# Kernel optimization log

Measured on AMD Instinct MI355X. Metric: run time of the kernel, lower is better.

The kernel has to match this reference:

```python
import jax, jax.numpy as jnp
import numpy as np


def setup_inputs() -> dict:
    key = jax.random.key(0)
    ks = jax.random.split(key, 4)
    B, T, I, H, O = 1024, 512, 64, 128, 10
    return {
        "x": jax.random.normal(ks[0], (B, T, I), dtype=jnp.float32),
        "W_hx": jax.random.normal(ks[1], (H, I), dtype=jnp.float32) * (6.0 / (H + I)) ** 0.5,
        "W_hh": jax.random.normal(ks[2], (H, H), dtype=jnp.float32) * (6.0 / (H + H)) ** 0.5,
        "b_hh": jnp.zeros((H,), dtype=jnp.float32),
        "W_ph": jax.random.normal(ks[3], (O, H), dtype=jnp.float32) * (6.0 / (O + H)) ** 0.5,
        "b_ph": jnp.zeros((O,), dtype=jnp.float32),
    }


def reference(x, W_hx, W_hh, b_hh, W_ph, b_ph):
    B, T, I = x.shape
    H = W_hh.shape[0]
    # Precompute input projections for all timesteps in one GEMM: [B,T,H]
    xproj = jnp.einsum("bti,hi->bth", x, W_hx)
    h0 = jnp.zeros((B, H), dtype=x.dtype)

    def step(h, xp_t):
        # xp_t: [B,H]; recurrent update h = tanh(W_hx x_t + W_hh h + b)
        h_new = jnp.tanh(xp_t + h @ W_hh.T + b_hh)
        return h_new, None

    # scan over time (leading axis): xproj transposed to [T,B,H]
    h_T, _ = jax.lax.scan(step, h0, jnp.swapaxes(xproj, 0, 1))
    return h_T @ W_ph.T + b_ph
```

## Files before the change

kernel.cpp:

```cpp
#include <hip/hip_runtime.h>
#include <math.h>


#define T_STEPS 512
#define I_DIM   64
#define H_DIM   128
#define O_DIM   10
#define BT      16
#define PITCH   136

typedef short  bf16x8 __attribute__((ext_vector_type(8)));
typedef float  f32x4  __attribute__((ext_vector_type(4)));

#define MFMA(A, Bi, C) __builtin_amdgcn_mfma_f32_16x16x32_bf16((A), __builtin_bit_cast(bf16x8, (Bi)), (C), 0, 0, 0)

static __device__ inline short f2bf(float f) {
    union { float f; unsigned u; } v; v.f = f;
    unsigned r = v.u + 0x7FFFu + ((v.u >> 16) & 1u);
    return (short)(r >> 16);
}
static __device__ inline unsigned rbf(float f) {
    return (__builtin_bit_cast(unsigned, f) + 0x8000u) >> 16;
}
static __device__ inline int pk2(float a, float b) {
    unsigned ua = __builtin_bit_cast(unsigned, a);
    unsigned ub = __builtin_bit_cast(unsigned, b);
    return (int)(((ua + 0x8000u) >> 16) | ((ub + 0x8000u) & 0xFFFF0000u));
}
static __device__ inline float bf2f(short s) {
    union { unsigned u; float f; } v; v.u = ((unsigned)(unsigned short)s) << 16;
    return v.f;
}

static __device__ inline void lds_barrier() {
    asm volatile("s_waitcnt lgkmcnt(0)\n\ts_barrier" ::: "memory");
}

#define RNN_STEP(P, XR, TN)                                                     \
    {                                                                           \
        const short* hb = hbuf[P] + c * PITCH + q * 8;                          \
        bf16x8 Ah0 = *(const bf16x8*)(hb +  0);                                 \
        bf16x8 Ah1 = *(const bf16x8*)(hb + 32);                                 \
        bf16x8 Ah2 = *(const bf16x8*)(hb + 64);                                 \
        bf16x8 Ah3 = *(const bf16x8*)(hb + 96);                                 \
        f32x4 Ca0 = Cxa0, Cb0 = Cxb0, Ca1 = Cxa1, Cb1 = Cxb1;                   \
        Ca0 = MFMA(Ah0, Bw[0][0], Ca0); Ca1 = MFMA(Ah0, Bw[1][0], Ca1);         \
        Cb0 = MFMA(Ah1, Bw[0][1], Cb0); Cb1 = MFMA(Ah1, Bw[1][1], Cb1);         \
        Ca0 = MFMA(Ah2, Bw[0][2], Ca0); Ca1 = MFMA(Ah2, Bw[1][2], Ca1);         \
        Cb0 = MFMA(Ah3, Bw[0][3], Cb0); Cb1 = MFMA(Ah3, Bw[1][3], Cb1);         \
        const f32x4 C0 = Ca0 + Cb0;                                             \
        const f32x4 C1 = Ca1 + Cb1;                                             \
        short* hw = hbuf[1 - (P)];                                              \
        _Pragma("unroll")                                                       \
        for (int r = 0; r < 4; ++r) {                                           \
            const int m = q * 4 + r;                                            \
            float s0 = C0[r] + bias0, s1 = C1[r] + bias1;                       \
            float e0 = __builtin_amdgcn_exp2f(s0 * 2.885390081777926825f);      \
            float e1 = __builtin_amdgcn_exp2f(s1 * 2.885390081777926825f);      \
            float h0 = fmaf(-2.0f, __builtin_amdgcn_rcpf(e0 + 1.0f), 1.0f);     \
            float h1 = fmaf(-2.0f, __builtin_amdgcn_rcpf(e1 + 1.0f), 1.0f);     \
            hw[m * PITCH + w * 32 + c]      = (short)rbf(h0);                   \
            hw[m * PITCH + w * 32 + 16 + c] = (short)rbf(h1);                   \
        }                                                                       \
         \
        {                                                                       \
            int4 axi0, axi1;                                                    \
            axi0.x = pk2(XR[0].x, XR[0].y); axi0.y = pk2(XR[0].z, XR[0].w);     \
            axi0.z = pk2(XR[1].x, XR[1].y); axi0.w = pk2(XR[1].z, XR[1].w);     \
            axi1.x = pk2(XR[2].x, XR[2].y); axi1.y = pk2(XR[2].z, XR[2].w);     \
            axi1.z = pk2(XR[3].x, XR[3].y); axi1.w = pk2(XR[3].z, XR[3].w);     \
            const int tn = ((TN) < T_STEPS) ? (TN) : (T_STEPS - 1);             \
            const float* pn = xrow + (size_t)tn * I_DIM;                        \
            XR[0] = *(const float4*)(pn +      q * 8);                          \
            XR[1] = *(const float4*)(pn +      q * 8 + 4);                      \
            XR[2] = *(const float4*)(pn + 32 + q * 8);                          \
            XR[3] = *(const float4*)(pn + 32 + q * 8 + 4);                      \
            bf16x8 Ax0 = __builtin_bit_cast(bf16x8, axi0);                      \
            bf16x8 Ax1 = __builtin_bit_cast(bf16x8, axi1);                      \
            const f32x4 Z = {0.f, 0.f, 0.f, 0.f};                               \
            Cxa0 = MFMA(Ax0, Bw[0][4], Z);                                      \
            Cxb0 = MFMA(Ax1, Bw[0][5], Z);                                      \
            Cxa1 = MFMA(Ax0, Bw[1][4], Z);                                      \
            Cxb1 = MFMA(Ax1, Bw[1][5], Z);                                      \
        }                                                                       \
        lds_barrier();                                                          \
    }

__global__ __launch_bounds__(256)
__attribute__((amdgpu_waves_per_eu(1, 2)))
void rnn_mfma_kernel(
    const float* __restrict__ x,
    const float* __restrict__ W_hx,
    const float* __restrict__ W_hh,
    const float* __restrict__ b_hh,
    const float* __restrict__ W_ph,
    const float* __restrict__ b_ph,
    float* __restrict__ out)
{
    const int b0   = blockIdx.x * BT;
    const int tid  = threadIdx.x;
    const int w    = tid >> 6;
    const int lane = tid & 63;
    const int c    = lane & 15;
    const int q    = lane >> 4;

    __shared__ short hbuf[2][BT * PITCH];

    int4 Bw[2][6];
    #pragma unroll
    for (int nt = 0; nt < 2; ++nt) {
        const int n = w * 32 + nt * 16 + c;
        #pragma unroll
        for (int kt = 0; kt < 6; ++kt) {
            const float* src = (kt < 4) ? (W_hh + n * H_DIM + kt * 32 + q * 8)
                                        : (W_hx + n * I_DIM + (kt - 4) * 32 + q * 8);
            short e[8];
            #pragma unroll
            for (int j = 0; j < 8; ++j) e[j] = f2bf(src[j]);
            Bw[nt][kt].x = ((int)(unsigned short)e[0]) | ((int)(unsigned short)e[1] << 16);
            Bw[nt][kt].y = ((int)(unsigned short)e[2]) | ((int)(unsigned short)e[3] << 16);
            Bw[nt][kt].z = ((int)(unsigned short)e[4]) | ((int)(unsigned short)e[5] << 16);
            Bw[nt][kt].w = ((int)(unsigned short)e[6]) | ((int)(unsigned short)e[7] << 16);
        }
    }
    #pragma unroll
    for (int nt = 0; nt < 2; ++nt)
        #pragma unroll
        for (int kt = 0; kt < 6; ++kt)
            asm volatile("" : "+v"(Bw[nt][kt].x), "+v"(Bw[nt][kt].y),
                              "+v"(Bw[nt][kt].z), "+v"(Bw[nt][kt].w));

    const float bias0 = b_hh[w * 32 + c];
    const float bias1 = b_hh[w * 32 + 16 + c];

    for (int idx = tid; idx < BT * PITCH; idx += 256) hbuf[0][idx] = 0;

    const float* xrow = x + (size_t)(b0 + c) * T_STEPS * I_DIM;
    float4 xrA[4], xrB[4];
    {
        const float* p0 = xrow;
        xrA[0] = *(const float4*)(p0 +      q * 8);
        xrA[1] = *(const float4*)(p0 +      q * 8 + 4);
        xrA[2] = *(const float4*)(p0 + 32 + q * 8);
        xrA[3] = *(const float4*)(p0 + 32 + q * 8 + 4);
        const float* p1 = xrow + I_DIM;
        xrB[0] = *(const float4*)(p1 +      q * 8);
        xrB[1] = *(const float4*)(p1 +      q * 8 + 4);
        xrB[2] = *(const float4*)(p1 + 32 + q * 8);
        xrB[3] = *(const float4*)(p1 + 32 + q * 8 + 4);
    }

    f32x4 Cxa0, Cxb0, Cxa1, Cxb1;
    {
        int4 axi0, axi1;
        axi0.x = pk2(xrA[0].x, xrA[0].y); axi0.y = pk2(xrA[0].z, xrA[0].w);
        axi0.z = pk2(xrA[1].x, xrA[1].y); axi0.w = pk2(xrA[1].z, xrA[1].w);
        axi1.x = pk2(xrA[2].x, xrA[2].y); axi1.y = pk2(xrA[2].z, xrA[2].w);
        axi1.z = pk2(xrA[3].x, xrA[3].y); axi1.w = pk2(xrA[3].z, xrA[3].w);
        const float* p2 = xrow + 2 * I_DIM;
        xrA[0] = *(const float4*)(p2 +      q * 8);
        xrA[1] = *(const float4*)(p2 +      q * 8 + 4);
        xrA[2] = *(const float4*)(p2 + 32 + q * 8);
        xrA[3] = *(const float4*)(p2 + 32 + q * 8 + 4);
        bf16x8 Ax0 = __builtin_bit_cast(bf16x8, axi0);
        bf16x8 Ax1 = __builtin_bit_cast(bf16x8, axi1);
        const f32x4 Z = {0.f, 0.f, 0.f, 0.f};
        Cxa0 = MFMA(Ax0, Bw[0][4], Z);
        Cxb0 = MFMA(Ax1, Bw[0][5], Z);
        Cxa1 = MFMA(Ax0, Bw[1][4], Z);
        Cxb1 = MFMA(Ax1, Bw[1][5], Z);
    }
    __syncthreads();

    #pragma unroll 1
    for (int t = 0; t < T_STEPS; t += 2) {
        RNN_STEP(0, xrB, t + 3)
        RNN_STEP(1, xrA, t + 4)
    }

    if (tid < BT * O_DIM) {
        const int m = tid / O_DIM;
        const int o = tid % O_DIM;
        float acc = b_ph[o];
        #pragma unroll 4
        for (int k = 0; k < H_DIM; ++k)
            acc = fmaf(W_ph[o * H_DIM + k], bf2f(hbuf[0][m * PITCH + k]), acc);
        out[(size_t)(b0 + m) * O_DIM + o] = acc;
    }
}

extern "C" void kernel_launch(void* const* d_in, const int* in_sizes, int n_in,
                              void* d_out, int out_size, void* d_ws, size_t ws_size,
                              hipStream_t stream) {
    const float* x    = (const float*)d_in[0];
    const float* W_hx = (const float*)d_in[1];
    const float* W_hh = (const float*)d_in[2];
    const float* b_hh = (const float*)d_in[3];
    const float* W_ph = (const float*)d_in[4];
    const float* b_ph = (const float*)d_in[5];
    float* out = (float*)d_out;

    rnn_mfma_kernel<<<1024 / BT, 256, 0, stream>>>(x, W_hx, W_hh, b_hh, W_ph, b_ph, out);
}
```

Before: 513.3 us.

## Split recurrence into producer/consumer waves and use Pade tanh

Doubles the block to 512 threads. Four producer waves load x, convert it to bf16 and compute the input projection plus bias with MFMA into a double-buffered LDS buffer one step ahead. Four consumer waves run only the recurrent W_hh MFMAs and the tanh, at raised priority. The tanh becomes a clamped Pade rational and the hidden-state stores are packed into pairs with a changed column mapping. This takes global loads and the input GEMM off the serial critical path, at the cost of extra LDS traffic and a larger barrier group, with the Pade approximation adding accuracy risk.

After: 463.6 us. 1.11x faster.

```diff
diff --git a/kernel.cpp b/kernel.cpp
--- a/kernel.cpp
+++ b/kernel.cpp
@@ -8,6 +8,7 @@
 #define O_DIM   10
 #define BT      16
 #define PITCH   136
+#define XPITCH  20
 
 typedef short  bf16x8 __attribute__((ext_vector_type(8)));
 typedef float  f32x4  __attribute__((ext_vector_type(4)));
@@ -19,9 +20,6 @@
     unsigned r = v.u + 0x7FFFu + ((v.u >> 16) & 1u);
     return (short)(r >> 16);
 }
-static __device__ inline unsigned rbf(float f) {
-    return (__builtin_bit_cast(unsigned, f) + 0x8000u) >> 16;
-}
 static __device__ inline int pk2(float a, float b) {
     unsigned ua = __builtin_bit_cast(unsigned, a);
     unsigned ub = __builtin_bit_cast(unsigned, b);
@@ -31,19 +29,39 @@
     union { unsigned u; float f; } v; v.u = ((unsigned)(unsigned short)s) << 16;
     return v.f;
 }
-
+static __device__ inline float pade_tanh(float z) {
+    const float t = z * z;
+    const float p = fmaf(fmaf(t + 378.0f, t, 17325.0f), t, 135135.0f);
+    const float qd = fmaf(fmaf(fmaf(28.0f, t, 3150.0f), t, 62370.0f), t, 135135.0f);
+    const float r = (z * p) * __builtin_amdgcn_rcpf(qd);
+    return __builtin_amdgcn_fmed3f(r, -1.0f, 1.0f);
+}
 static __device__ inline void lds_barrier() {
     asm volatile("s_waitcnt lgkmcnt(0)\n\ts_barrier" ::: "memory");
 }
-
-#define RNN_STEP(P, XR, TN)                                                     \
+static __device__ inline int4 load_frag(const float* src) {
+    short e[8];
+    #pragma unroll
+    for (int j = 0; j < 8; ++j) e[j] = f2bf(src[j]);
+    int4 r;
+    r.x = ((int)(unsigned short)e[0]) | ((int)(unsigned short)e[1] << 16);
+    r.y = ((int)(unsigned short)e[2]) | ((int)(unsigned short)e[3] << 16);
+    r.z = ((int)(unsigned short)e[4]) | ((int)(unsigned short)e[5] << 16);
+    r.w = ((int)(unsigned short)e[6]) | ((int)(unsigned short)e[7] << 16);
+    return r;
+}
+
+#define CONS_STEP(P)                                                            \
     {                                                                           \
         const short* hb = hbuf[P] + c * PITCH + q * 8;                          \
         bf16x8 Ah0 = *(const bf16x8*)(hb +  0);                                 \
         bf16x8 Ah1 = *(const bf16x8*)(hb + 32);                                 \
         bf16x8 Ah2 = *(const bf16x8*)(hb + 64);                                 \
         bf16x8 Ah3 = *(const bf16x8*)(hb + 96);                                 \
-        f32x4 Ca0 = Cxa0, Cb0 = Cxb0, Ca1 = Cxa1, Cb1 = Cxb1;                   \
+        f32x4 Ca0 = *(const f32x4*)&xpb[P][ n0      * XPITCH + 4 * q];          \
+        f32x4 Ca1 = *(const f32x4*)&xpb[P][(n0 + 1) * XPITCH + 4 * q];          \
+        f32x4 Cb0 = {0.f, 0.f, 0.f, 0.f};                                       \
+        f32x4 Cb1 = {0.f, 0.f, 0.f, 0.f};                                       \
         Ca0 = MFMA(Ah0, Bw[0][0], Ca0); Ca1 = MFMA(Ah0, Bw[1][0], Ca1);         \
         Cb0 = MFMA(Ah1, Bw[0][1], Cb0); Cb1 = MFMA(Ah1, Bw[1][1], Cb1);         \
         Ca0 = MFMA(Ah2, Bw[0][2], Ca0); Ca1 = MFMA(Ah2, Bw[1][2], Ca1);         \
@@ -54,40 +72,36 @@
         _Pragma("unroll")                                                       \
         for (int r = 0; r < 4; ++r) {                                           \
             const int m = q * 4 + r;                                            \
-            float s0 = C0[r] + bias0, s1 = C1[r] + bias1;                       \
-            float e0 = __builtin_amdgcn_exp2f(s0 * 2.885390081777926825f);      \
-            float e1 = __builtin_amdgcn_exp2f(s1 * 2.885390081777926825f);      \
-            float h0 = fmaf(-2.0f, __builtin_amdgcn_rcpf(e0 + 1.0f), 1.0f);     \
-            float h1 = fmaf(-2.0f, __builtin_amdgcn_rcpf(e1 + 1.0f), 1.0f);     \
-            hw[m * PITCH + w * 32 + c]      = (short)rbf(h0);                   \
-            hw[m * PITCH + w * 32 + 16 + c] = (short)rbf(h1);                   \
+            const float h0 = pade_tanh(C0[r]);                                  \
+            const float h1 = pade_tanh(C1[r]);                                  \
+            *(int*)(hw + m * PITCH + n0) = pk2(h0, h1);                         \
         }                                                                       \
-         \
-        {                                                                       \
-            int4 axi0, axi1;                                                    \
-            axi0.x = pk2(XR[0].x, XR[0].y); axi0.y = pk2(XR[0].z, XR[0].w);     \
-            axi0.z = pk2(XR[1].x, XR[1].y); axi0.w = pk2(XR[1].z, XR[1].w);     \
-            axi1.x = pk2(XR[2].x, XR[2].y); axi1.y = pk2(XR[2].z, XR[2].w);     \
-            axi1.z = pk2(XR[3].x, XR[3].y); axi1.w = pk2(XR[3].z, XR[3].w);     \
-            const int tn = ((TN) < T_STEPS) ? (TN) : (T_STEPS - 1);             \
-            const float* pn = xrow + (size_t)tn * I_DIM;                        \
-            XR[0] = *(const float4*)(pn +      q * 8);                          \
-            XR[1] = *(const float4*)(pn +      q * 8 + 4);                      \
-            XR[2] = *(const float4*)(pn + 32 + q * 8);                          \
-            XR[3] = *(const float4*)(pn + 32 + q * 8 + 4);                      \
-            bf16x8 Ax0 = __builtin_bit_cast(bf16x8, axi0);                      \
-            bf16x8 Ax1 = __builtin_bit_cast(bf16x8, axi1);                      \
-            const f32x4 Z = {0.f, 0.f, 0.f, 0.f};                               \
-            Cxa0 = MFMA(Ax0, Bw[0][4], Z);                                      \
-            Cxb0 = MFMA(Ax1, Bw[0][5], Z);                                      \
-            Cxa1 = MFMA(Ax0, Bw[1][4], Z);                                      \
-            Cxb1 = MFMA(Ax1, Bw[1][5], Z);                                      \
-        }                                                                       \
-        lds_barrier();                                                          \
-    }
-
-__global__ __launch_bounds__(256)
-__attribute__((amdgpu_waves_per_eu(1, 2)))
+    }
+
+#define PROD_STEP(P, XR, TN)                                                    \
+    {                                                                           \
+        int4 a0, a1;                                                            \
+        a0.x = pk2(XR[0].x, XR[0].y); a0.y = pk2(XR[0].z, XR[0].w);             \
+        a0.z = pk2(XR[1].x, XR[1].y); a0.w = pk2(XR[1].z, XR[1].w);             \
+        a1.x = pk2(XR[2].x, XR[2].y); a1.y = pk2(XR[2].z, XR[2].w);             \
+        a1.z = pk2(XR[3].x, XR[3].y); a1.w = pk2(XR[3].z, XR[3].w);             \
+        const int tn = ((TN) < T_STEPS) ? (TN) : (T_STEPS - 1);                 \
+        const float* pn = xrow + (size_t)tn * I_DIM;                            \
+        XR[0] = *(const float4*)(pn +      q * 8);                              \
+        XR[1] = *(const float4*)(pn +      q * 8 + 4);                          \
+        XR[2] = *(const float4*)(pn + 32 + q * 8);                              \
+        XR[3] = *(const float4*)(pn + 32 + q * 8 + 4);                          \
+        bf16x8 Ax0 = __builtin_bit_cast(bf16x8, a0);                            \
+        bf16x8 Ax1 = __builtin_bit_cast(bf16x8, a1);                            \
+        f32x4 P0 = MFMA(Ax0, BX[0][0], biasv[0]);                               \
+        P0 = MFMA(Ax1, BX[0][1], P0);                                           \
+        f32x4 P1 = MFMA(Ax0, BX[1][0], biasv[1]);                               \
+        P1 = MFMA(Ax1, BX[1][1], P1);                                           \
+        *(f32x4*)&xpb[1 - (P)][ n0      * XPITCH + 4 * q] = P0;                 \
+        *(f32x4*)&xpb[1 - (P)][(n0 + 1) * XPITCH + 4 * q] = P1;                 \
+    }
+
+__global__ __launch_bounds__(512, 2)
 void rnn_mfma_kernel(
     const float* __restrict__ x,
     const float* __restrict__ W_hx,
@@ -99,83 +113,99 @@
 {
     const int b0   = blockIdx.x * BT;
     const int tid  = threadIdx.x;
-    const int w    = tid >> 6;
+    const int wave = tid >> 6;
     const int lane = tid & 63;
     const int c    = lane & 15;
     const int q    = lane >> 4;
-
-    __shared__ short hbuf[2][BT * PITCH];
-
-    int4 Bw[2][6];
-    #pragma unroll
-    for (int nt = 0; nt < 2; ++nt) {
-        const int n = w * 32 + nt * 16 + c;
-        #pragma unroll
-        for (int kt = 0; kt < 6; ++kt) {
-            const float* src = (kt < 4) ? (W_hh + n * H_DIM + kt * 32 + q * 8)
-                                        : (W_hx + n * I_DIM + (kt - 4) * 32 + q * 8);
-            short e[8];
-            #pragma unroll
-            for (int j = 0; j < 8; ++j) e[j] = f2bf(src[j]);
-            Bw[nt][kt].x = ((int)(unsigned short)e[0]) | ((int)(unsigned short)e[1] << 16);
-            Bw[nt][kt].y = ((int)(unsigned short)e[2]) | ((int)(unsigned short)e[3] << 16);
-            Bw[nt][kt].z = ((int)(unsigned short)e[4]) | ((int)(unsigned short)e[5] << 16);
-            Bw[nt][kt].w = ((int)(unsigned short)e[6]) | ((int)(unsigned short)e[7] << 16);
-        }
-    }
-    #pragma unroll
-    for (int nt = 0; nt < 2; ++nt)
-        #pragma unroll
-        for (int kt = 0; kt < 6; ++kt)
-            asm volatile("" : "+v"(Bw[nt][kt].x), "+v"(Bw[nt][kt].y),
-                              "+v"(Bw[nt][kt].z), "+v"(Bw[nt][kt].w));
-
-    const float bias0 = b_hh[w * 32 + c];
-    const float bias1 = b_hh[w * 32 + 16 + c];
-
-    for (int idx = tid; idx < BT * PITCH; idx += 256) hbuf[0][idx] = 0;
-
-    const float* xrow = x + (size_t)(b0 + c) * T_STEPS * I_DIM;
-    float4 xrA[4], xrB[4];
-    {
-        const float* p0 = xrow;
-        xrA[0] = *(const float4*)(p0 +      q * 8);
-        xrA[1] = *(const float4*)(p0 +      q * 8 + 4);
-        xrA[2] = *(const float4*)(p0 + 32 + q * 8);
-        xrA[3] = *(const float4*)(p0 + 32 + q * 8 + 4);
+    const int w    = wave & 3;
+    const int n0   = w * 32 + 2 * c;
+
+    __shared__ __align__(16) short hbuf[2][BT * PITCH];
+    __shared__ __align__(16) float xpb[2][H_DIM * XPITCH];
+
+    for (int idx = tid; idx < BT * PITCH; idx += 512) hbuf[0][idx] = 0;
+
+    if (wave < 4) {
+        int4 Bw[2][4];
+        #pragma unroll
+        for (int nt = 0; nt < 2; ++nt)
+            #pragma unroll
+            for (int kt = 0; kt < 4; ++kt)
+                Bw[nt][kt] = load_frag(W_hh + (n0 + nt) * H_DIM + kt * 32 + q * 8);
+        #pragma unroll
+        for (int nt = 0; nt < 2; ++nt)
+            #pragma unroll
+            for (int kt = 0; kt < 4; ++kt)
+                asm volatile("" : "+v"(Bw[nt][kt].x), "+v"(Bw[nt][kt].y),
+                                  "+v"(Bw[nt][kt].z), "+v"(Bw[nt][kt].w));
+        __syncthreads();
+        __builtin_amdgcn_s_setprio(1);
+        #pragma unroll 1
+        for (int t = 0; t < T_STEPS; t += 2) {
+            CONS_STEP(0)
+            lds_barrier();
+            CONS_STEP(1)
+            lds_barrier();
+        }
+        __builtin_amdgcn_s_setprio(0);
+    } else {
+        int4 BX[2][2];
+        f32x4 biasv[2];
+        #pragma unroll
+        for (int nt = 0; nt < 2; ++nt) {
+            #pragma unroll
+            for (int kx = 0; kx < 2; ++kx)
+                BX[nt][kx] = load_frag(W_hx + (n0 + nt) * I_DIM + kx * 32 + q * 8);
+            const float bb = b_hh[n0 + nt];
+            biasv[nt] = (f32x4){bb, bb, bb, bb};
+        }
+        #pragma unroll
+        for (int nt = 0; nt < 2; ++nt)
+            #pragma unroll
+            for (int kx = 0; kx < 2; ++kx)
+                asm volatile("" : "+v"(BX[nt][kx].x), "+v"(BX[nt][kx].y),
+                                  "+v"(BX[nt][kx].z), "+v"(BX[nt][kx].w));
+
+        const float* xrow = x + (size_t)(b0 + c) * T_STEPS * I_DIM;
+        {
+            float4 x0[4];
+            x0[0] = *(const float4*)(xrow +      q * 8);
+            x0[1] = *(const float4*)(xrow +      q * 8 + 4);
+            x0[2] = *(const float4*)(xrow + 32 + q * 8);
+            x0[3] = *(const float4*)(xrow + 32 + q * 8 + 4);
+            int4 a0, a1;
+            a0.x = pk2(x0[0].x, x0[0].y); a0.y = pk2(x0[0].z, x0[0].w);
+            a0.z = pk2(x0[1].x, x0[1].y); a0.w = pk2(x0[1].z, x0[1].w);
+            a1.x = pk2(x0[2].x, x0[2].y); a1.y = pk2(x0[2].z, x0[2].w);
+            a1.z = pk2(x0[3].x, x0[3].y); a1.w = pk2(x0[3].z, x0[3].w);
+            bf16x8 Ax0 = __builtin_bit_cast(bf16x8, a0);
+            bf16x8 Ax1 = __builtin_bit_cast(bf16x8, a1);
+            f32x4 P0 = MFMA(Ax0, BX[0][0], biasv[0]);
+            P0 = MFMA(Ax1, BX[0][1], P0);
+            f32x4 P1 = MFMA(Ax0, BX[1][0], biasv[1]);
+            P1 = MFMA(Ax1, BX[1][1], P1);
+            *(f32x4*)&xpb[0][ n0      * XPITCH + 4 * q] = P0;
+            *(f32x4*)&xpb[0][(n0 + 1) * XPITCH + 4 * q] = P1;
+        }
+        float4 xrA[4], xrB[4];
         const float* p1 = xrow + I_DIM;
-        xrB[0] = *(const float4*)(p1 +      q * 8);
-        xrB[1] = *(const float4*)(p1 +      q * 8 + 4);
-        xrB[2] = *(const float4*)(p1 + 32 + q * 8);
-        xrB[3] = *(const float4*)(p1 + 32 + q * 8 + 4);
-    }
-
-    f32x4 Cxa0, Cxb0, Cxa1, Cxb1;
-    {
-        int4 axi0, axi1;
-        axi0.x = pk2(xrA[0].x, xrA[0].y); axi0.y = pk2(xrA[0].z, xrA[0].w);
-        axi0.z = pk2(xrA[1].x, xrA[1].y); axi0.w = pk2(xrA[1].z, xrA[1].w);
-        axi1.x = pk2(xrA[2].x, xrA[2].y); axi1.y = pk2(xrA[2].z, xrA[2].w);
-        axi1.z = pk2(xrA[3].x, xrA[3].y); axi1.w = pk2(xrA[3].z, xrA[3].w);
+        xrA[0] = *(const float4*)(p1 +      q * 8);
+        xrA[1] = *(const float4*)(p1 +      q * 8 + 4);
+        xrA[2] = *(const float4*)(p1 + 32 + q * 8);
+        xrA[3] = *(const float4*)(p1 + 32 + q * 8 + 4);
         const float* p2 = xrow + 2 * I_DIM;
-        xrA[0] = *(const float4*)(p2 +      q * 8);
-        xrA[1] = *(const float4*)(p2 +      q * 8 + 4);
-        xrA[2] = *(const float4*)(p2 + 32 + q * 8);
-        xrA[3] = *(const float4*)(p2 + 32 + q * 8 + 4);
-        bf16x8 Ax0 = __builtin_bit_cast(bf16x8, axi0);
-        bf16x8 Ax1 = __builtin_bit_cast(bf16x8, axi1);
-        const f32x4 Z = {0.f, 0.f, 0.f, 0.f};
-        Cxa0 = MFMA(Ax0, Bw[0][4], Z);
-        Cxb0 = MFMA(Ax1, Bw[0][5], Z);
-        Cxa1 = MFMA(Ax0, Bw[1][4], Z);
-        Cxb1 = MFMA(Ax1, Bw[1][5], Z);
-    }
-    __syncthreads();
-
-    #pragma unroll 1
-    for (int t = 0; t < T_STEPS; t += 2) {
-        RNN_STEP(0, xrB, t + 3)
-        RNN_STEP(1, xrA, t + 4)
+        xrB[0] = *(const float4*)(p2 +      q * 8);
+        xrB[1] = *(const float4*)(p2 +      q * 8 + 4);
+        xrB[2] = *(const float4*)(p2 + 32 + q * 8);
+        xrB[3] = *(const float4*)(p2 + 32 + q * 8 + 4);
+        __syncthreads();
+        #pragma unroll 1
+        for (int t = 0; t < T_STEPS; t += 2) {
+            PROD_STEP(0, xrA, t + 3)
+            lds_barrier();
+            PROD_STEP(1, xrB, t + 4)
+            lds_barrier();
+        }
     }
 
     if (tid < BT * O_DIM) {
@@ -200,5 +230,5 @@
     const float* b_ph = (const float*)d_in[5];
     float* out = (float*)d_out;
 
-    rnn_mfma_kernel<<<1024 / BT, 256, 0, stream>>>(x, W_hx, W_hh, b_hh, W_ph, b_ph, out);
-}
+    rnn_mfma_kernel<<<1024 / BT, 512, 0, stream>>>(x, W_hx, W_hh, b_hh, W_ph, b_ph, out);
+}
```

## Run each batch tile's recurrence in one wave without barriers

Applied to the files above, without the earlier changes.

Each 16-row batch tile is now handled by a single 64-lane wave instead of four waves. That one wave holds all 128 hidden columns of W_hh and W_hx as bf16 register fragments and runs the whole 48-MFMA step itself. This removes the per-step workgroup barrier and the double-buffered LDS hidden state, leaving one buffer and an lgkmcnt wait. Bias is folded into the MFMA accumulator init, and hidden outputs are interleaved so each lane writes packed bf16 pairs. The cost is that the matrix work and tanh work per step are serialized on one SIMD with very high register use.

New measurement: 806.5 us. 1.57x slower.

```diff
diff --git a/kernel.cpp b/kernel.cpp
--- a/kernel.cpp
+++ b/kernel.cpp
@@ -12,16 +12,14 @@
 typedef short  bf16x8 __attribute__((ext_vector_type(8)));
 typedef float  f32x4  __attribute__((ext_vector_type(4)));
 
-#define MFMA(A, Bi, C) __builtin_amdgcn_mfma_f32_16x16x32_bf16((A), __builtin_bit_cast(bf16x8, (Bi)), (C), 0, 0, 0)
+#define MFMA(A, Bi, C) __builtin_amdgcn_mfma_f32_16x16x32_bf16(                 \
+    __builtin_bit_cast(bf16x8, (A)), __builtin_bit_cast(bf16x8, (Bi)), (C), 0, 0, 0)
 
 static __device__ inline short f2bf(float f) {
     union { float f; unsigned u; } v; v.f = f;
     unsigned r = v.u + 0x7FFFu + ((v.u >> 16) & 1u);
     return (short)(r >> 16);
 }
-static __device__ inline unsigned rbf(float f) {
-    return (__builtin_bit_cast(unsigned, f) + 0x8000u) >> 16;
-}
 static __device__ inline int pk2(float a, float b) {
     unsigned ua = __builtin_bit_cast(unsigned, a);
     unsigned ub = __builtin_bit_cast(unsigned, b);
@@ -31,63 +29,78 @@
     union { unsigned u; float f; } v; v.u = ((unsigned)(unsigned short)s) << 16;
     return v.f;
 }
-
-static __device__ inline void lds_barrier() {
-    asm volatile("s_waitcnt lgkmcnt(0)\n\ts_barrier" ::: "memory");
-}
-
-#define RNN_STEP(P, XR, TN)                                                     \
+static __device__ inline float tanh_fast(float z) {
+    float e = __builtin_amdgcn_exp2f(z * 2.885390081777926825f);
+    return fmaf(-2.0f, __builtin_amdgcn_rcpf(e + 1.0f), 1.0f);
+}
+static __device__ inline int4 load_frag(const float* src) {
+    short e[8];
+    #pragma unroll
+    for (int j = 0; j < 8; ++j) e[j] = f2bf(src[j]);
+    int4 r;
+    r.x = ((int)(unsigned short)e[0]) | ((int)(unsigned short)e[1] << 16);
+    r.y = ((int)(unsigned short)e[2]) | ((int)(unsigned short)e[3] << 16);
+    r.z = ((int)(unsigned short)e[4]) | ((int)(unsigned short)e[5] << 16);
+    r.w = ((int)(unsigned short)e[6]) | ((int)(unsigned short)e[7] << 16);
+    return r;
+}
+static __device__ inline void lds_fence() {
+    asm volatile("s_waitcnt lgkmcnt(0)" ::: "memory");
+    __builtin_amdgcn_sched_barrier(0);
+}
+
+#define RNN_STEP(XR, TN)                                                        \
     {                                                                           \
-        const short* hb = hbuf[P] + c * PITCH + q * 8;                          \
+        const short* hb = hbuf + c * PITCH + q * 8;                             \
         bf16x8 Ah0 = *(const bf16x8*)(hb +  0);                                 \
         bf16x8 Ah1 = *(const bf16x8*)(hb + 32);                                 \
         bf16x8 Ah2 = *(const bf16x8*)(hb + 64);                                 \
         bf16x8 Ah3 = *(const bf16x8*)(hb + 96);                                 \
-        f32x4 Ca0 = Cxa0, Cb0 = Cxb0, Ca1 = Cxa1, Cb1 = Cxb1;                   \
-        Ca0 = MFMA(Ah0, Bw[0][0], Ca0); Ca1 = MFMA(Ah0, Bw[1][0], Ca1);         \
-        Cb0 = MFMA(Ah1, Bw[0][1], Cb0); Cb1 = MFMA(Ah1, Bw[1][1], Cb1);         \
-        Ca0 = MFMA(Ah2, Bw[0][2], Ca0); Ca1 = MFMA(Ah2, Bw[1][2], Ca1);         \
-        Cb0 = MFMA(Ah3, Bw[0][3], Cb0); Cb1 = MFMA(Ah3, Bw[1][3], Cb1);         \
-        const f32x4 C0 = Ca0 + Cb0;                                             \
-        const f32x4 C1 = Ca1 + Cb1;                                             \
-        short* hw = hbuf[1 - (P)];                                              \
+        f32x4 C[4][2];                                                          \
         _Pragma("unroll")                                                       \
-        for (int r = 0; r < 4; ++r) {                                           \
-            const int m = q * 4 + r;                                            \
-            float s0 = C0[r] + bias0, s1 = C1[r] + bias1;                       \
-            float e0 = __builtin_amdgcn_exp2f(s0 * 2.885390081777926825f);      \
-            float e1 = __builtin_amdgcn_exp2f(s1 * 2.885390081777926825f);      \
-            float h0 = fmaf(-2.0f, __builtin_amdgcn_rcpf(e0 + 1.0f), 1.0f);     \
-            float h1 = fmaf(-2.0f, __builtin_amdgcn_rcpf(e1 + 1.0f), 1.0f);     \
-            hw[m * PITCH + w * 32 + c]      = (short)rbf(h0);                   \
-            hw[m * PITCH + w * 32 + 16 + c] = (short)rbf(h1);                   \
+        for (int np = 0; np < 4; ++np) {                                        \
+            _Pragma("unroll")                                                   \
+            for (int sub = 0; sub < 2; ++sub) {                                 \
+                C[np][sub] = MFMA(AXF[0], BW[np][sub][4], biasC4[np][sub]);     \
+                C[np][sub] = MFMA(AXF[1], BW[np][sub][5], C[np][sub]);          \
+                C[np][sub] = MFMA(Ah0, BW[np][sub][0], C[np][sub]);             \
+                C[np][sub] = MFMA(Ah1, BW[np][sub][1], C[np][sub]);             \
+                C[np][sub] = MFMA(Ah2, BW[np][sub][2], C[np][sub]);             \
+                C[np][sub] = MFMA(Ah3, BW[np][sub][3], C[np][sub]);             \
+            }                                                                   \
         }                                                                       \
-         \
+        _Pragma("unroll")                                                       \
+        for (int np = 0; np < 4; ++np) {                                        \
+            _Pragma("unroll")                                                   \
+            for (int r = 0; r < 4; ++r) {                                       \
+                const int m = q * 4 + r;                                        \
+                const float h0 = tanh_fast(C[np][0][r]);                        \
+                const float h1 = tanh_fast(C[np][1][r]);                        \
+                *(int*)(hbuf + m * PITCH + 32 * np + 2 * c) = pk2(h0, h1);      \
+            }                                                                   \
+        }                                                                       \
+        lds_fence();                                                            \
+        AXF[0] = pack4(XR[0], XR[1]);                                           \
+        AXF[1] = pack4(XR[2], XR[3]);                                           \
         {                                                                       \
-            int4 axi0, axi1;                                                    \
-            axi0.x = pk2(XR[0].x, XR[0].y); axi0.y = pk2(XR[0].z, XR[0].w);     \
-            axi0.z = pk2(XR[1].x, XR[1].y); axi0.w = pk2(XR[1].z, XR[1].w);     \
-            axi1.x = pk2(XR[2].x, XR[2].y); axi1.y = pk2(XR[2].z, XR[2].w);     \
-            axi1.z = pk2(XR[3].x, XR[3].y); axi1.w = pk2(XR[3].z, XR[3].w);     \
             const int tn = ((TN) < T_STEPS) ? (TN) : (T_STEPS - 1);             \
             const float* pn = xrow + (size_t)tn * I_DIM;                        \
             XR[0] = *(const float4*)(pn +      q * 8);                          \
             XR[1] = *(const float4*)(pn +      q * 8 + 4);                      \
             XR[2] = *(const float4*)(pn + 32 + q * 8);                          \
             XR[3] = *(const float4*)(pn + 32 + q * 8 + 4);                      \
-            bf16x8 Ax0 = __builtin_bit_cast(bf16x8, axi0);                      \
-            bf16x8 Ax1 = __builtin_bit_cast(bf16x8, axi1);                      \
-            const f32x4 Z = {0.f, 0.f, 0.f, 0.f};                               \
-            Cxa0 = MFMA(Ax0, Bw[0][4], Z);                                      \
-            Cxb0 = MFMA(Ax1, Bw[0][5], Z);                                      \
-            Cxa1 = MFMA(Ax0, Bw[1][4], Z);                                      \
-            Cxb1 = MFMA(Ax1, Bw[1][5], Z);                                      \
         }                                                                       \
-        lds_barrier();                                                          \
-    }
-
-__global__ __launch_bounds__(256)
-__attribute__((amdgpu_waves_per_eu(1, 2)))
+    }
+
+static __device__ inline int4 pack4(const float4 a, const float4 b) {
+    int4 r;
+    r.x = pk2(a.x, a.y); r.y = pk2(a.z, a.w);
+    r.z = pk2(b.x, b.y); r.w = pk2(b.z, b.w);
+    return r;
+}
+
+__global__ __launch_bounds__(64, 1)
+__attribute__((amdgpu_waves_per_eu(1, 1)))
 void rnn_mfma_kernel(
     const float* __restrict__ x,
     const float* __restrict__ W_hx,
@@ -99,92 +112,81 @@
 {
     const int b0   = blockIdx.x * BT;
     const int tid  = threadIdx.x;
-    const int w    = tid >> 6;
     const int lane = tid & 63;
     const int c    = lane & 15;
     const int q    = lane >> 4;
 
-    __shared__ short hbuf[2][BT * PITCH];
-
-    int4 Bw[2][6];
+    __shared__ __align__(16) short hbuf[BT * PITCH];
+
+    int4 BW[4][2][6];
+    f32x4 biasC4[4][2];
     #pragma unroll
-    for (int nt = 0; nt < 2; ++nt) {
-        const int n = w * 32 + nt * 16 + c;
+    for (int np = 0; np < 4; ++np) {
         #pragma unroll
-        for (int kt = 0; kt < 6; ++kt) {
-            const float* src = (kt < 4) ? (W_hh + n * H_DIM + kt * 32 + q * 8)
-                                        : (W_hx + n * I_DIM + (kt - 4) * 32 + q * 8);
-            short e[8];
+        for (int sub = 0; sub < 2; ++sub) {
+            const int n = 32 * np + 2 * c + sub;
             #pragma unroll
-            for (int j = 0; j < 8; ++j) e[j] = f2bf(src[j]);
-            Bw[nt][kt].x = ((int)(unsigned short)e[0]) | ((int)(unsigned short)e[1] << 16);
-            Bw[nt][kt].y = ((int)(unsigned short)e[2]) | ((int)(unsigned short)e[3] << 16);
-            Bw[nt][kt].z = ((int)(unsigned short)e[4]) | ((int)(unsigned short)e[5] << 16);
-            Bw[nt][kt].w = ((int)(unsigned short)e[6]) | ((int)(unsigned short)e[7] << 16);
+            for (int kt = 0; kt < 6; ++kt) {
+                const float* src = (kt < 4) ? (W_hh + n * H_DIM + kt * 32 + q * 8)
+                                            : (W_hx + n * I_DIM + (kt - 4) * 32 + q * 8);
+                BW[np][sub][kt] = load_frag(src);
+            }
+            const float bb = b_hh[n];
+            biasC4[np][sub] = (f32x4){bb, bb, bb, bb};
         }
     }
     #pragma unroll
-    for (int nt = 0; nt < 2; ++nt)
+    for (int np = 0; np < 4; ++np)
         #pragma unroll
-        for (int kt = 0; kt < 6; ++kt)
-            asm volatile("" : "+v"(Bw[nt][kt].x), "+v"(Bw[nt][kt].y),
-                              "+v"(Bw[nt][kt].z), "+v"(Bw[nt][kt].w));
-
-    const float bias0 = b_hh[w * 32 + c];
-    const float bias1 = b_hh[w * 32 + 16 + c];
-
-    for (int idx = tid; idx < BT * PITCH; idx += 256) hbuf[0][idx] = 0;
+        for (int sub = 0; sub < 2; ++sub) {
+            #pragma unroll
+            for (int kt = 0; kt < 6; ++kt)
+                asm volatile("" : "+v"(BW[np][sub][kt].x), "+v"(BW[np][sub][kt].y),
+                                  "+v"(BW[np][sub][kt].z), "+v"(BW[np][sub][kt].w));
+            asm volatile("" : "+v"(biasC4[np][sub]));
+        }
+
+    for (int idx = tid; idx < BT * PITCH; idx += 64) hbuf[idx] = 0;
+    lds_fence();
 
     const float* xrow = x + (size_t)(b0 + c) * T_STEPS * I_DIM;
+    int4 AXF[2];
+    {
+        float4 x0[4];
+        x0[0] = *(const float4*)(xrow +      q * 8);
+        x0[1] = *(const float4*)(xrow +      q * 8 + 4);
+        x0[2] = *(const float4*)(xrow + 32 + q * 8);
+        x0[3] = *(const float4*)(xrow + 32 + q * 8 + 4);
+        AXF[0] = pack4(x0[0], x0[1]);
+        AXF[1] = pack4(x0[2], x0[3]);
+    }
     float4 xrA[4], xrB[4];
     {
-        const float* p0 = xrow;
-        xrA[0] = *(const float4*)(p0 +      q * 8);
-        xrA[1] = *(const float4*)(p0 +      q * 8 + 4);
-        xrA[2] = *(const float4*)(p0 + 32 + q * 8);
-        xrA[3] = *(const float4*)(p0 + 32 + q * 8 + 4);
         const float* p1 = xrow + I_DIM;
-        xrB[0] = *(const float4*)(p1 +      q * 8);
-        xrB[1] = *(const float4*)(p1 +      q * 8 + 4);
-        xrB[2] = *(const float4*)(p1 + 32 + q * 8);
-        xrB[3] = *(const float4*)(p1 + 32 + q * 8 + 4);
-    }
-
-    f32x4 Cxa0, Cxb0, Cxa1, Cxb1;
-    {
-        int4 axi0, axi1;
-        axi0.x = pk2(xrA[0].x, xrA[0].y); axi0.y = pk2(xrA[0].z, xrA[0].w);
-        axi0.z = pk2(xrA[1].x, xrA[1].y); axi0.w = pk2(xrA[1].z, xrA[1].w);
-        axi1.x = pk2(xrA[2].x, xrA[2].y); axi1.y = pk2(xrA[2].z, xrA[2].w);
-        axi1.z = pk2(xrA[3].x, xrA[3].y); axi1.w = pk2(xrA[3].z, xrA[3].w);
+        xrA[0] = *(const float4*)(p1 +      q * 8);
+        xrA[1] = *(const float4*)(p1 +      q * 8 + 4);
+        xrA[2] = *(const float4*)(p1 + 32 + q * 8);
+        xrA[3] = *(const float4*)(p1 + 32 + q * 8 + 4);
         const float* p2 = xrow + 2 * I_DIM;
-        xrA[0] = *(const float4*)(p2 +      q * 8);
-        xrA[1] = *(const float4*)(p2 +      q * 8 + 4);
-        xrA[2] = *(const float4*)(p2 + 32 + q * 8);
-        xrA[3] = *(const float4*)(p2 + 32 + q * 8 + 4);
-        bf16x8 Ax0 = __builtin_bit_cast(bf16x8, axi0);
-        bf16x8 Ax1 = __builtin_bit_cast(bf16x8, axi1);
-        const f32x4 Z = {0.f, 0.f, 0.f, 0.f};
-        Cxa0 = MFMA(Ax0, Bw[0][4], Z);
-        Cxb0 = MFMA(Ax1, Bw[0][5], Z);
-        Cxa1 = MFMA(Ax0, Bw[1][4], Z);
-        Cxb1 = MFMA(Ax1, Bw[1][5], Z);
-    }
-    __syncthreads();
+        xrB[0] = *(const float4*)(p2 +      q * 8);
+        xrB[1] = *(const float4*)(p2 +      q * 8 + 4);
+        xrB[2] = *(const float4*)(p2 + 32 + q * 8);
+        xrB[3] = *(const float4*)(p2 + 32 + q * 8 + 4);
+    }
 
     #pragma unroll 1
     for (int t = 0; t < T_STEPS; t += 2) {
-        RNN_STEP(0, xrB, t + 3)
-        RNN_STEP(1, xrA, t + 4)
-    }
-
-    if (tid < BT * O_DIM) {
-        const int m = tid / O_DIM;
-        const int o = tid % O_DIM;
+        RNN_STEP(xrA, t + 3)
+        RNN_STEP(xrB, t + 4)
+    }
+
+    for (int idx = tid; idx < BT * O_DIM; idx += 64) {
+        const int m = idx / O_DIM;
+        const int o = idx % O_DIM;
         float acc = b_ph[o];
         #pragma unroll 4
         for (int k = 0; k < H_DIM; ++k)
-            acc = fmaf(W_ph[o * H_DIM + k], bf2f(hbuf[0][m * PITCH + k]), acc);
+            acc = fmaf(W_ph[o * H_DIM + k], bf2f(hbuf[m * PITCH + k]), acc);
         out[(size_t)(b0 + m) * O_DIM + o] = acc;
     }
 }
@@ -200,5 +202,5 @@
     const float* b_ph = (const float*)d_in[5];
     float* out = (float*)d_out;
 
-    rnn_mfma_kernel<<<1024 / BT, 256, 0, stream>>>(x, W_hx, W_hh, b_hh, W_ph, b_ph, out);
-}
+    rnn_mfma_kernel<<<1024 / BT, 64, 0, stream>>>(x, W_hx, W_hh, b_hh, W_ph, b_ph, out);
+}
```

## Pack two batch chunks per block, use rational tanh and packed h stores

Applied to the files above, without the earlier changes.

Each block now runs two independent 16-row batch chunks with 8 waves, which halves the grid to 32 blocks of 512 threads sharing one barrier per step. Tanh is replaced by a Padé rational approximation clamped with med3, using a single reciprocal shared by two outputs instead of two exp2 and two rcp. The column mapping is permuted so each lane writes two adjacent bf16 h values as one packed 32-bit LDS store. The bias is folded into the input-projection MFMA accumulator. Halving the block count leaves more CUs idle, the shared barrier couples the two chunks, and the Padé form loses accuracy for larger pre-activations.

New measurement: 657.5 us. +28.1%, slower.

```diff
diff --git a/kernel.cpp b/kernel.cpp
--- a/kernel.cpp
+++ b/kernel.cpp
@@ -7,21 +7,20 @@
 #define H_DIM   128
 #define O_DIM   10
 #define BT      16
+#define NCH     2
 #define PITCH   136
 
 typedef short  bf16x8 __attribute__((ext_vector_type(8)));
 typedef float  f32x4  __attribute__((ext_vector_type(4)));
 
-#define MFMA(A, Bi, C) __builtin_amdgcn_mfma_f32_16x16x32_bf16((A), __builtin_bit_cast(bf16x8, (Bi)), (C), 0, 0, 0)
+#define MFMA(A, Bi, C) __builtin_amdgcn_mfma_f32_16x16x32_bf16(                 \
+    __builtin_bit_cast(bf16x8, (A)), __builtin_bit_cast(bf16x8, (Bi)), (C), 0, 0, 0)
 
 static __device__ inline short f2bf(float f) {
     union { float f; unsigned u; } v; v.f = f;
     unsigned r = v.u + 0x7FFFu + ((v.u >> 16) & 1u);
     return (short)(r >> 16);
 }
-static __device__ inline unsigned rbf(float f) {
-    return (__builtin_bit_cast(unsigned, f) + 0x8000u) >> 16;
-}
 static __device__ inline int pk2(float a, float b) {
     unsigned ua = __builtin_bit_cast(unsigned, a);
     unsigned ub = __builtin_bit_cast(unsigned, b);
@@ -31,63 +30,80 @@
     union { unsigned u; float f; } v; v.u = ((unsigned)(unsigned short)s) << 16;
     return v.f;
 }
-
+static __device__ inline int4 load_frag(const float* src) {
+    short e[8];
+    #pragma unroll
+    for (int j = 0; j < 8; ++j) e[j] = f2bf(src[j]);
+    int4 r;
+    r.x = ((int)(unsigned short)e[0]) | ((int)(unsigned short)e[1] << 16);
+    r.y = ((int)(unsigned short)e[2]) | ((int)(unsigned short)e[3] << 16);
+    r.z = ((int)(unsigned short)e[4]) | ((int)(unsigned short)e[5] << 16);
+    r.w = ((int)(unsigned short)e[6]) | ((int)(unsigned short)e[7] << 16);
+    return r;
+}
+static __device__ inline int4 pack4(const float4 a, const float4 b) {
+    int4 r;
+    r.x = pk2(a.x, a.y); r.y = pk2(a.z, a.w);
+    r.z = pk2(b.x, b.y); r.w = pk2(b.z, b.w);
+    return r;
+}
 static __device__ inline void lds_barrier() {
     asm volatile("s_waitcnt lgkmcnt(0)\n\ts_barrier" ::: "memory");
 }
 
 #define RNN_STEP(P, XR, TN)                                                     \
     {                                                                           \
-        const short* hb = hbuf[P] + c * PITCH + q * 8;                          \
+        const short* hb = hsrc[P] + c * PITCH + q * 8;                          \
         bf16x8 Ah0 = *(const bf16x8*)(hb +  0);                                 \
         bf16x8 Ah1 = *(const bf16x8*)(hb + 32);                                 \
         bf16x8 Ah2 = *(const bf16x8*)(hb + 64);                                 \
         bf16x8 Ah3 = *(const bf16x8*)(hb + 96);                                 \
-        f32x4 Ca0 = Cxa0, Cb0 = Cxb0, Ca1 = Cxa1, Cb1 = Cxb1;                   \
-        Ca0 = MFMA(Ah0, Bw[0][0], Ca0); Ca1 = MFMA(Ah0, Bw[1][0], Ca1);         \
-        Cb0 = MFMA(Ah1, Bw[0][1], Cb0); Cb1 = MFMA(Ah1, Bw[1][1], Cb1);         \
-        Ca0 = MFMA(Ah2, Bw[0][2], Ca0); Ca1 = MFMA(Ah2, Bw[1][2], Ca1);         \
-        Cb0 = MFMA(Ah3, Bw[0][3], Cb0); Cb1 = MFMA(Ah3, Bw[1][3], Cb1);         \
+        f32x4 Ca0 = Cx0, Ca1 = Cx1;                                             \
+        f32x4 Cb0 = {0.f, 0.f, 0.f, 0.f};                                       \
+        f32x4 Cb1 = {0.f, 0.f, 0.f, 0.f};                                       \
+        Ca0 = MFMA(Ah0, BW[0][0], Ca0); Ca1 = MFMA(Ah0, BW[1][0], Ca1);         \
+        Cb0 = MFMA(Ah1, BW[0][1], Cb0); Cb1 = MFMA(Ah1, BW[1][1], Cb1);         \
+        Ca0 = MFMA(Ah2, BW[0][2], Ca0); Ca1 = MFMA(Ah2, BW[1][2], Ca1);         \
+        Cb0 = MFMA(Ah3, BW[0][3], Cb0); Cb1 = MFMA(Ah3, BW[1][3], Cb1);         \
         const f32x4 C0 = Ca0 + Cb0;                                             \
         const f32x4 C1 = Ca1 + Cb1;                                             \
-        short* hw = hbuf[1 - (P)];                                              \
+        short* hw = hsrc[1 - (P)];                                              \
         _Pragma("unroll")                                                       \
         for (int r = 0; r < 4; ++r) {                                           \
             const int m = q * 4 + r;                                            \
-            float s0 = C0[r] + bias0, s1 = C1[r] + bias1;                       \
-            float e0 = __builtin_amdgcn_exp2f(s0 * 2.885390081777926825f);      \
-            float e1 = __builtin_amdgcn_exp2f(s1 * 2.885390081777926825f);      \
-            float h0 = fmaf(-2.0f, __builtin_amdgcn_rcpf(e0 + 1.0f), 1.0f);     \
-            float h1 = fmaf(-2.0f, __builtin_amdgcn_rcpf(e1 + 1.0f), 1.0f);     \
-            hw[m * PITCH + w * 32 + c]      = (short)rbf(h0);                   \
-            hw[m * PITCH + w * 32 + 16 + c] = (short)rbf(h1);                   \
+            const float z0 = C0[r], z1 = C1[r];                                 \
+            const float t0 = z0 * z0, t1 = z1 * z1;                             \
+            const float p0 = fmaf(fmaf(t0 + 378.f, t0, 17325.f), t0, 135135.f); \
+            const float p1 = fmaf(fmaf(t1 + 378.f, t1, 17325.f), t1, 135135.f); \
+            const float q0 = fmaf(fmaf(fmaf(28.f, t0, 3150.f), t0, 62370.f), t0, 135135.f); \
+            const float q1 = fmaf(fmaf(fmaf(28.f, t1, 3150.f), t1, 62370.f), t1, 135135.f); \
+            const float rr = __builtin_amdgcn_rcpf(q0 * q1);                    \
+            const float h0 = __builtin_amdgcn_fmed3f(z0 * p0 * (rr * q1), -1.f, 1.f); \
+            const float h1 = __builtin_amdgcn_fmed3f(z1 * p1 * (rr * q0), -1.f, 1.f); \
+            *(int*)(hw + m * PITCH + n0) = pk2(h0, h1);                         \
         }                                                                       \
-         \
+                     \
         {                                                                       \
-            int4 axi0, axi1;                                                    \
-            axi0.x = pk2(XR[0].x, XR[0].y); axi0.y = pk2(XR[0].z, XR[0].w);     \
-            axi0.z = pk2(XR[1].x, XR[1].y); axi0.w = pk2(XR[1].z, XR[1].w);     \
-            axi1.x = pk2(XR[2].x, XR[2].y); axi1.y = pk2(XR[2].z, XR[2].w);     \
-            axi1.z = pk2(XR[3].x, XR[3].y); axi1.w = pk2(XR[3].z, XR[3].w);     \
+            int4 ax0, ax1;                                                      \
+            ax0.x = pk2(XR[0].x, XR[0].y); ax0.y = pk2(XR[0].z, XR[0].w);       \
+            ax0.z = pk2(XR[1].x, XR[1].y); ax0.w = pk2(XR[1].z, XR[1].w);       \
+            ax1.x = pk2(XR[2].x, XR[2].y); ax1.y = pk2(XR[2].z, XR[2].w);       \
+            ax1.z = pk2(XR[3].x, XR[3].y); ax1.w = pk2(XR[3].z, XR[3].w);       \
             const int tn = ((TN) < T_STEPS) ? (TN) : (T_STEPS - 1);             \
             const float* pn = xrow + (size_t)tn * I_DIM;                        \
             XR[0] = *(const float4*)(pn +      q * 8);                          \
             XR[1] = *(const float4*)(pn +      q * 8 + 4);                      \
             XR[2] = *(const float4*)(pn + 32 + q * 8);                          \
             XR[3] = *(const float4*)(pn + 32 + q * 8 + 4);                      \
-            bf16x8 Ax0 = __builtin_bit_cast(bf16x8, axi0);                      \
-            bf16x8 Ax1 = __builtin_bit_cast(bf16x8, axi1);                      \
-            const f32x4 Z = {0.f, 0.f, 0.f, 0.f};                               \
-            Cxa0 = MFMA(Ax0, Bw[0][4], Z);                                      \
-            Cxb0 = MFMA(Ax1, Bw[0][5], Z);                                      \
-            Cxa1 = MFMA(Ax0, Bw[1][4], Z);                                      \
-            Cxb1 = MFMA(Ax1, Bw[1][5], Z);                                      \
+            Cx0 = MFMA(ax0, BW[0][4], biasv[0]);                                \
+            Cx0 = MFMA(ax1, BW[0][5], Cx0);                                     \
+            Cx1 = MFMA(ax0, BW[1][4], biasv[1]);                                \
+            Cx1 = MFMA(ax1, BW[1][5], Cx1);                                     \
         }                                                                       \
         lds_barrier();                                                          \
     }
 
-__global__ __launch_bounds__(256)
-__attribute__((amdgpu_waves_per_eu(1, 2)))
+__global__ __launch_bounds__(512, 2)
 void rnn_mfma_kernel(
     const float* __restrict__ x,
     const float* __restrict__ W_hx,
@@ -97,43 +113,46 @@
     const float* __restrict__ b_ph,
     float* __restrict__ out)
 {
-    const int b0   = blockIdx.x * BT;
     const int tid  = threadIdx.x;
-    const int w    = tid >> 6;
+    const int wave = tid >> 6;
+    const int g    = wave >> 2;
+    const int w    = wave & 3;
     const int lane = tid & 63;
     const int c    = lane & 15;
     const int q    = lane >> 4;
-
-    __shared__ short hbuf[2][BT * PITCH];
-
-    int4 Bw[2][6];
+    const int n0   = w * 32 + 2 * c;
+    const int b0   = blockIdx.x * (BT * NCH) + g * BT;
+
+    __shared__ __align__(16) short hbuf[NCH][2][BT * PITCH];
+    short* hsrc[2] = { hbuf[g][0], hbuf[g][1] };
+
+    int4 BW[2][6];
+    f32x4 biasv[2];
     #pragma unroll
-    for (int nt = 0; nt < 2; ++nt) {
-        const int n = w * 32 + nt * 16 + c;
+    for (int sub = 0; sub < 2; ++sub) {
+        const int n = n0 + sub;
         #pragma unroll
         for (int kt = 0; kt < 6; ++kt) {
             const float* src = (kt < 4) ? (W_hh + n * H_DIM + kt * 32 + q * 8)
                                         : (W_hx + n * I_DIM + (kt - 4) * 32 + q * 8);
-            short e[8];
-            #pragma unroll
-            for (int j = 0; j < 8; ++j) e[j] = f2bf(src[j]);
-            Bw[nt][kt].x = ((int)(unsigned short)e[0]) | ((int)(unsigned short)e[1] << 16);
-            Bw[nt][kt].y = ((int)(unsigned short)e[2]) | ((int)(unsigned short)e[3] << 16);
-            Bw[nt][kt].z = ((int)(unsigned short)e[4]) | ((int)(unsigned short)e[5] << 16);
-            Bw[nt][kt].w = ((int)(unsigned short)e[6]) | ((int)(unsigned short)e[7] << 16);
+            BW[sub][kt] = load_frag(src);
         }
+        const float bb = b_hh[n];
+        biasv[sub] = (f32x4){bb, bb, bb, bb};
     }
     #pragma unroll
-    for (int nt = 0; nt < 2; ++nt)
+    for (int sub = 0; sub < 2; ++sub) {
         #pragma unroll
         for (int kt = 0; kt < 6; ++kt)
-            asm volatile("" : "+v"(Bw[nt][kt].x), "+v"(Bw[nt][kt].y),
-                              "+v"(Bw[nt][kt].z), "+v"(Bw[nt][kt].w));
-
-    const float bias0 = b_hh[w * 32 + c];
-    const float bias1 = b_hh[w * 32 + 16 + c];
-
-    for (int idx = tid; idx < BT * PITCH; idx += 256) hbuf[0][idx] = 0;
+            asm volatile("" : "+v"(BW[sub][kt].x), "+v"(BW[sub][kt].y),
+                              "+v"(BW[sub][kt].z), "+v"(BW[sub][kt].w));
+        asm volatile("" : "+v"(biasv[sub]));
+    }
+
+    for (int idx = tid; idx < NCH * BT * PITCH; idx += 512)
+        hbuf[0][0][idx % (BT * PITCH) + (idx / (BT * PITCH)) * 0] = 0;
+    for (int idx = tid; idx < NCH * 2 * BT * PITCH; idx += 512)
+        ((short*)hbuf)[idx] = 0;
 
     const float* xrow = x + (size_t)(b0 + c) * T_STEPS * I_DIM;
     float4 xrA[4], xrB[4];
@@ -150,25 +169,20 @@
         xrB[3] = *(const float4*)(p1 + 32 + q * 8 + 4);
     }
 
-    f32x4 Cxa0, Cxb0, Cxa1, Cxb1;
+    f32x4 Cx0, Cx1;
     {
-        int4 axi0, axi1;
-        axi0.x = pk2(xrA[0].x, xrA[0].y); axi0.y = pk2(xrA[0].z, xrA[0].w);
-        axi0.z = pk2(xrA[1].x, xrA[1].y); axi0.w = pk2(xrA[1].z, xrA[1].w);
-        axi1.x = pk2(xrA[2].x, xrA[2].y); axi1.y = pk2(xrA[2].z, xrA[2].w);
-        axi1.z = pk2(xrA[3].x, xrA[3].y); axi1.w = pk2(xrA[3].z, xrA[3].w);
+        int4 ax0, ax1;
+        ax0 = pack4(xrA[0], xrA[1]);
+        ax1 = pack4(xrA[2], xrA[3]);
         const float* p2 = xrow + 2 * I_DIM;
         xrA[0] = *(const float4*)(p2 +      q * 8);
         xrA[1] = *(const float4*)(p2 +      q * 8 + 4);
         xrA[2] = *(const float4*)(p2 + 32 + q * 8);
         xrA[3] = *(const float4*)(p2 + 32 + q * 8 + 4);
-        bf16x8 Ax0 = __builtin_bit_cast(bf16x8, axi0);
-        bf16x8 Ax1 = __builtin_bit_cast(bf16x8, axi1);
-        const f32x4 Z = {0.f, 0.f, 0.f, 0.f};
-        Cxa0 = MFMA(Ax0, Bw[0][4], Z);
-        Cxb0 = MFMA(Ax1, Bw[0][5], Z);
-        Cxa1 = MFMA(Ax0, Bw[1][4], Z);
-        Cxb1 = MFMA(Ax1, Bw[1][5], Z);
+        Cx0 = MFMA(ax0, BW[0][4], biasv[0]);
+        Cx0 = MFMA(ax1, BW[0][5], Cx0);
+        Cx1 = MFMA(ax0, BW[1][4], biasv[1]);
+        Cx1 = MFMA(ax1, BW[1][5], Cx1);
     }
     __syncthreads();
 
@@ -178,14 +192,15 @@
         RNN_STEP(1, xrA, t + 4)
     }
 
-    if (tid < BT * O_DIM) {
-        const int m = tid / O_DIM;
-        const int o = tid % O_DIM;
+    if (tid < NCH * BT * O_DIM) {
+        const int m32 = tid / O_DIM;
+        const int o   = tid % O_DIM;
+        const short* hrow = hbuf[m32 >> 4][0] + (m32 & 15) * PITCH;
         float acc = b_ph[o];
         #pragma unroll 4
         for (int k = 0; k < H_DIM; ++k)
-            acc = fmaf(W_ph[o * H_DIM + k], bf2f(hbuf[0][m * PITCH + k]), acc);
-        out[(size_t)(b0 + m) * O_DIM + o] = acc;
+            acc = fmaf(W_ph[o * H_DIM + k], bf2f(hrow[k]), acc);
+        out[(size_t)(blockIdx.x * (BT * NCH) + m32) * O_DIM + o] = acc;
     }
 }
 
@@ -200,5 +215,5 @@
     const float* b_ph = (const float*)d_in[5];
     float* out = (float*)d_out;
 
-    rnn_mfma_kernel<<<1024 / BT, 256, 0, stream>>>(x, W_hx, W_hh, b_hh, W_ph, b_ph, out);
-}
+    rnn_mfma_kernel<<<1024 / (BT * NCH), 512, 0, stream>>>(x, W_hx, W_hh, b_hh, W_ph, b_ph, out);
+}
```
